# Kernel optimization log

Hardware: AMD Instinct MI355X
Metric: run time of the kernel (lower is better)

The kernel has to match this reference:

```python
import jax, jax.numpy as jnp
import numpy as np

TEMPERATURE = 0.05
EPS = 1e-8  # torch.cosine_similarity eps


def setup_inputs() -> dict:
    key = jax.random.key(0)
    k1, k2 = jax.random.split(key)
    N, D = 8192, 256
    text_embeddings = jax.random.normal(k1, (N, D), dtype=jnp.float32)
    text_pos_embeddings = jax.random.normal(k2, (N, D), dtype=jnp.float32)
    return {"text_embeddings": text_embeddings, "text_pos_embeddings": text_pos_embeddings}


def reference(text_embeddings, text_pos_embeddings):
    # cosine similarity via normalize + single GEMM (same math as broadcasted
    # torch.cosine_similarity, which clamps norms at eps)
    a_norm = jnp.maximum(jnp.linalg.norm(text_embeddings, axis=-1, keepdims=True), EPS)
    b_norm = jnp.maximum(jnp.linalg.norm(text_pos_embeddings, axis=-1, keepdims=True), EPS)
    a = text_embeddings / a_norm  # [N, D]
    b = text_pos_embeddings / b_norm  # [N, D]
    sim = jnp.einsum("nd,md->nm", a, b) / TEMPERATURE  # [N, N]
    # cross-entropy with labels = arange(N): mean over rows of -log_softmax diag
    logp = jax.nn.log_softmax(sim, axis=-1)
    loss = -jnp.mean(jnp.diagonal(logp))
    return loss
```

## Files before the change

kernel.cpp:

```cpp
#include <hip/hip_runtime.h>
#include <hip/hip_bf16.h>
#include <math.h>

#define DIM 256

typedef float f32x4 __attribute__((ext_vector_type(4)));
typedef int   i32x8 __attribute__((ext_vector_type(8)));

__constant__ const float kTempInvLog2e = 20.0f * 1.4426950408889634f;
#define LN2 0.6931471805599453f
#define EPS_NORM 1e-8f
#define SCALE_ONE 0x7F7F7F7Fu

static __device__ inline unsigned f2fp8x4(float4 v, float s) {
    int r = 0;
    r = __builtin_amdgcn_cvt_pk_fp8_f32(v.x * s, v.y * s, r, false);
    r = __builtin_amdgcn_cvt_pk_fp8_f32(v.z * s, v.w * s, r, true);
    return (unsigned)r;
}

static __device__ inline i32x8 ld_frag32(const void* p0, const void* p1) {
    uint4 a = *(const uint4*)p0;
    uint4 b = *(const uint4*)p1;
    i32x8 v;
    v[0] = a.x; v[1] = a.y; v[2] = a.z; v[3] = a.w;
    v[4] = b.x; v[5] = b.y; v[6] = b.z; v[7] = b.w;
    return v;
}

__global__ __launch_bounds__(256) void normpack_kernel(
    const float* __restrict__ A, const float* __restrict__ B,
    unsigned char* __restrict__ Apk, unsigned char* __restrict__ Bpk,
    float* __restrict__ diag, int n)
{
    __shared__ uint4 lA[256];
    __shared__ uint4 lB[256];
    const int t = threadIdx.x;
    const int rl = t >> 4;
    const int c16 = t & 15;
    const int r = blockIdx.x * 16 + rl;

    const float4* pa = (const float4*)(A + (size_t)r * DIM + c16 * 16);
    const float4* pb = (const float4*)(B + (size_t)r * DIM + c16 * 16);
    float4 a0 = pa[0], a1 = pa[1], a2 = pa[2], a3 = pa[3];
    float4 b0 = pb[0], b1 = pb[1], b2 = pb[2], b3 = pb[3];

    float ssa = a0.x*a0.x + a0.y*a0.y + a0.z*a0.z + a0.w*a0.w
              + a1.x*a1.x + a1.y*a1.y + a1.z*a1.z + a1.w*a1.w
              + a2.x*a2.x + a2.y*a2.y + a2.z*a2.z + a2.w*a2.w
              + a3.x*a3.x + a3.y*a3.y + a3.z*a3.z + a3.w*a3.w;
    float ssb = b0.x*b0.x + b0.y*b0.y + b0.z*b0.z + b0.w*b0.w
              + b1.x*b1.x + b1.y*b1.y + b1.z*b1.z + b1.w*b1.w
              + b2.x*b2.x + b2.y*b2.y + b2.z*b2.z + b2.w*b2.w
              + b3.x*b3.x + b3.y*b3.y + b3.z*b3.z + b3.w*b3.w;
    float dd  = a0.x*b0.x + a0.y*b0.y + a0.z*b0.z + a0.w*b0.w
              + a1.x*b1.x + a1.y*b1.y + a1.z*b1.z + a1.w*b1.w
              + a2.x*b2.x + a2.y*b2.y + a2.z*b2.z + a2.w*b2.w
              + a3.x*b3.x + a3.y*b3.y + a3.z*b3.z + a3.w*b3.w;
#pragma unroll
    for (int m = 1; m < 16; m <<= 1) {
        ssa += __shfl_xor(ssa, m, 64);
        ssb += __shfl_xor(ssb, m, 64);
        dd  += __shfl_xor(dd, m, 64);
    }
    float na = fmaxf(sqrtf(ssa), EPS_NORM);
    float nb = fmaxf(sqrtf(ssb), EPS_NORM);
    float sa = kTempInvLog2e / na;
    float sb = 1.0f / nb;
    if (c16 == 0) diag[r] = dd / (na * nb) * kTempInvLog2e;

    const int u = ((c16 >> 3) << 7) + ((c16 & 1) << 6) + rl + ((c16 & 7) >> 1) * 16;
    uint4 ga, gb;
    ga.x = f2fp8x4(a0, sa); ga.y = f2fp8x4(a1, sa);
    ga.z = f2fp8x4(a2, sa); ga.w = f2fp8x4(a3, sa);
    gb.x = f2fp8x4(b0, sb); gb.y = f2fp8x4(b1, sb);
    gb.z = f2fp8x4(b2, sb); gb.w = f2fp8x4(b3, sb);
    lA[u] = ga; lB[u] = gb;
    __syncthreads();

    ((uint4*)Apk)[(size_t)blockIdx.x * 256 + t] = lA[t];
    ((uint4*)Bpk)[(size_t)blockIdx.x * 256 + t] = lB[t];
}

static __device__ inline void async_copy16(const void* g, void* l) {
    __builtin_amdgcn_global_load_lds(
        (const __attribute__((address_space(1))) unsigned int*)g,
        (__attribute__((address_space(3))) unsigned int*)l, 16, 0, 0);
}

__global__ __launch_bounds__(256, 2) void gemm_lse_kernel(
    const unsigned char* __restrict__ Apk, const unsigned char* __restrict__ Bpk,
    float* __restrict__ partial, int n)
{
    __shared__ char ldsbuf[32768];
    const int lane = threadIdx.x & 63;
    const int w = threadIdx.x >> 6;
    const int c = lane & 15;
    const int q = lane >> 4;

    const int i = blockIdx.x;
    const int split = ((i & 7) << 1) | ((i >> 3) & 1);
    const int rowblk = i >> 4;
    const int rowbase = rowblk * 256 + w * 64;

    i32x8 afrag[4][2];
#pragma unroll
    for (int m = 0; m < 4; ++m) {
        const int AT = rowblk * 16 + w * 4 + m;
#pragma unroll
        for (int kc = 0; kc < 2; ++kc) {
            const char* base = (const char*)Apk + ((size_t)AT * 2 + kc) * 2048 + lane * 16;
            afrag[m][kc] = ld_frag32(base, base + 1024);
        }
    }
#pragma unroll
    for (int m = 0; m < 4; ++m)
#pragma unroll
        for (int kc = 0; kc < 2; ++kc)
            asm volatile("" : "+v"(afrag[m][kc]));

    float sums[16];
#pragma unroll
    for (int s = 0; s < 16; ++s) sums[s] = 0.0f;

    const char* bbase = (const char*)Bpk + (size_t)split * 32 * 4096;
    const int niter = 8;

    {
        const char* src = bbase + w * 4096 + (size_t)lane * 16;
        char* dst = ldsbuf + w * 4096;
#pragma unroll
        for (int j = 0; j < 4; ++j)
            async_copy16(src + j * 1024, dst + j * 1024);
    }
    __syncthreads();

    for (int it = 0; it < niter; ++it) {
        const int cur = it & 1;
        if (it + 1 < niter) {
            const char* src = bbase + (size_t)(it + 1) * 16384 + w * 4096 + (size_t)lane * 16;
            char* dst = ldsbuf + (cur ^ 1) * 16384 + w * 4096;
#pragma unroll
            for (int j = 0; j < 4; ++j)
                async_copy16(src + j * 1024, dst + j * 1024);
        }

        f32x4 acc[4][4];
#pragma unroll
        for (int m = 0; m < 4; ++m)
#pragma unroll
            for (int nc = 0; nc < 4; ++nc)
                acc[m][nc] = (f32x4){0.f, 0.f, 0.f, 0.f};

        const char* lb = ldsbuf + cur * 16384 + (size_t)lane * 16;
#pragma unroll
        for (int nc = 0; nc < 4; ++nc) {
#pragma unroll
            for (int kc = 0; kc < 2; ++kc) {
                const char* p = lb + nc * 4096 + kc * 2048;
                i32x8 bfrag = ld_frag32(p, p + 1024);
#pragma unroll
                for (int m = 0; m < 4; ++m)
                    acc[m][nc] = __builtin_amdgcn_mfma_scale_f32_16x16x128_f8f6f4(
                        afrag[m][kc], bfrag, acc[m][nc],
                        0, 0,
                        0, SCALE_ONE,
                        0, SCALE_ONE);
            }
        }

#pragma unroll
        for (int m = 0; m < 4; ++m)
#pragma unroll
            for (int nc = 0; nc < 4; ++nc)
#pragma unroll
                for (int r = 0; r < 4; ++r)
                    sums[m * 4 + r] += __builtin_amdgcn_exp2f(acc[m][nc][r]);

        __syncthreads();
    }

#pragma unroll
    for (int s = 0; s < 16; ++s) {
        float v = sums[s];
        v += __shfl_xor(v, 1, 64);
        v += __shfl_xor(v, 2, 64);
        v += __shfl_xor(v, 4, 64);
        v += __shfl_xor(v, 8, 64);
        sums[s] = v;
    }
    if (c == 0) {
#pragma unroll
        for (int m = 0; m < 4; ++m)
#pragma unroll
            for (int r = 0; r < 4; ++r)
                partial[(size_t)(rowbase + m * 16 + q * 4 + r) * 16 + split] = sums[m * 4 + r];
    }
}

__global__ __launch_bounds__(1024) void finale_kernel(
    const float* __restrict__ partial, const float* __restrict__ diag,
    float* __restrict__ out, int n)
{
    __shared__ float red[1024];
    float local = 0.0f;
    for (int row = threadIdx.x; row < n; row += 1024) {
        const float4* p = (const float4*)(partial + (size_t)row * 16);
        float4 p0 = p[0], p1 = p[1], p2 = p[2], p3 = p[3];
        float s = (p0.x + p0.y + p0.z + p0.w) + (p1.x + p1.y + p1.z + p1.w)
                + (p2.x + p2.y + p2.z + p2.w) + (p3.x + p3.y + p3.z + p3.w);
        local += log2f(s) - diag[row];
    }
    red[threadIdx.x] = local;
    __syncthreads();
    for (int off = 512; off > 0; off >>= 1) {
        if (threadIdx.x < off) red[threadIdx.x] += red[threadIdx.x + off];
        __syncthreads();
    }
    if (threadIdx.x == 0) out[0] = red[0] * (LN2 / (float)n);
}

extern "C" void kernel_launch(void* const* d_in, const int* in_sizes, int n_in,
                              void* d_out, int out_size, void* d_ws, size_t ws_size,
                              hipStream_t stream) {
    const int n = in_sizes[0] / DIM;
    const float* A = (const float*)d_in[0];
    const float* B = (const float*)d_in[1];
    float* out = (float*)d_out;

    unsigned char* Apk = (unsigned char*)d_ws;
    unsigned char* Bpk = Apk + (size_t)n * DIM;
    float* partial = (float*)(Bpk + (size_t)n * DIM);
    float* diag = partial + (size_t)n * 16;

    normpack_kernel<<<n / 16, 256, 0, stream>>>(A, B, Apk, Bpk, diag, n);

    gemm_lse_kernel<<<(n / 256) * 16, 256, 0, stream>>>(Apk, Bpk, partial, n);

    finale_kernel<<<1, 1024, 0, stream>>>(partial, diag, out, n);
}
```

Before: 96.22 us.

## Split columns into 32 blocks, load whole B tile into LDS once

The GEMM grid is doubled so each block covers 256 columns instead of 512. The block copies its full 64KB B slice into LDS with a single async load and one barrier, replacing the double-buffered loop with its per-iteration syncs. The A-fragment loads are issued after the B copy so the two overlap. This gives more blocks and fewer barriers, at the cost of 64KB LDS per block, which may cap occupancy at 2 blocks per CU, and a wider partial buffer for the finale to reduce.

```diff
diff --git a/kernel.cpp b/kernel.cpp
--- a/kernel.cpp
+++ b/kernel.cpp
@@ -92,16 +92,24 @@
     const unsigned char* __restrict__ Apk, const unsigned char* __restrict__ Bpk,
     float* __restrict__ partial, int n)
 {
-    __shared__ char ldsbuf[32768];
+    __shared__ char ldsbuf[65536];
     const int lane = threadIdx.x & 63;
     const int w = threadIdx.x >> 6;
     const int c = lane & 15;
     const int q = lane >> 4;
 
     const int i = blockIdx.x;
-    const int split = ((i & 7) << 1) | ((i >> 3) & 1);
-    const int rowblk = i >> 4;
+    const int colblk = ((i & 7) << 2) | ((i >> 3) & 3);
+    const int rowblk = i >> 5;
     const int rowbase = rowblk * 256 + w * 64;
+
+    {
+        const char* src = (const char*)Bpk + (size_t)colblk * 65536 + w * 16384 + (size_t)lane * 16;
+        char* dst = ldsbuf + w * 16384;
+#pragma unroll
+        for (int j = 0; j < 16; ++j)
+            async_copy16(src + j * 1024, dst + j * 1024);
+    }
 
     i32x8 afrag[4][2];
 #pragma unroll
@@ -123,61 +131,31 @@
 #pragma unroll
     for (int s = 0; s < 16; ++s) sums[s] = 0.0f;
 
-    const char* bbase = (const char*)Bpk + (size_t)split * 32 * 4096;
-    const int niter = 8;
-
-    {
-        const char* src = bbase + w * 4096 + (size_t)lane * 16;
-        char* dst = ldsbuf + w * 4096;
-#pragma unroll
-        for (int j = 0; j < 4; ++j)
-            async_copy16(src + j * 1024, dst + j * 1024);
-    }
     __syncthreads();
 
-    for (int it = 0; it < niter; ++it) {
-        const int cur = it & 1;
-        if (it + 1 < niter) {
-            const char* src = bbase + (size_t)(it + 1) * 16384 + w * 4096 + (size_t)lane * 16;
-            char* dst = ldsbuf + (cur ^ 1) * 16384 + w * 4096;
-#pragma unroll
-            for (int j = 0; j < 4; ++j)
-                async_copy16(src + j * 1024, dst + j * 1024);
+    const char* lb = ldsbuf + (size_t)lane * 16;
+#pragma unroll 4
+    for (int nc = 0; nc < 16; ++nc) {
+        f32x4 acc[4];
+#pragma unroll
+        for (int m = 0; m < 4; ++m) acc[m] = (f32x4){0.f, 0.f, 0.f, 0.f};
+#pragma unroll
+        for (int kc = 0; kc < 2; ++kc) {
+            const char* p = lb + nc * 4096 + kc * 2048;
+            i32x8 bfrag = ld_frag32(p, p + 1024);
+#pragma unroll
+            for (int m = 0; m < 4; ++m)
+                acc[m] = __builtin_amdgcn_mfma_scale_f32_16x16x128_f8f6f4(
+                    afrag[m][kc], bfrag, acc[m],
+                    0, 0,
+                    0, SCALE_ONE,
+                    0, SCALE_ONE);
         }
-
-        f32x4 acc[4][4];
 #pragma unroll
         for (int m = 0; m < 4; ++m)
 #pragma unroll
-            for (int nc = 0; nc < 4; ++nc)
-                acc[m][nc] = (f32x4){0.f, 0.f, 0.f, 0.f};
-
-        const char* lb = ldsbuf + cur * 16384 + (size_t)lane * 16;
-#pragma unroll
-        for (int nc = 0; nc < 4; ++nc) {
-#pragma unroll
-            for (int kc = 0; kc < 2; ++kc) {
-                const char* p = lb + nc * 4096 + kc * 2048;
-                i32x8 bfrag = ld_frag32(p, p + 1024);
-#pragma unroll
-                for (int m = 0; m < 4; ++m)
-                    acc[m][nc] = __builtin_amdgcn_mfma_scale_f32_16x16x128_f8f6f4(
-                        afrag[m][kc], bfrag, acc[m][nc],
-                        0, 0,
-                        0, SCALE_ONE,
-                        0, SCALE_ONE);
-            }
-        }
-
-#pragma unroll
-        for (int m = 0; m < 4; ++m)
-#pragma unroll
-            for (int nc = 0; nc < 4; ++nc)
-#pragma unroll
-                for (int r = 0; r < 4; ++r)
-                    sums[m * 4 + r] += __builtin_amdgcn_exp2f(acc[m][nc][r]);
-
-        __syncthreads();
+            for (int r = 0; r < 4; ++r)
+                sums[m * 4 + r] += __builtin_amdgcn_exp2f(acc[m][r]);
     }
 
 #pragma unroll
@@ -194,7 +172,7 @@
         for (int m = 0; m < 4; ++m)
 #pragma unroll
             for (int r = 0; r < 4; ++r)
-                partial[(size_t)(rowbase + m * 16 + q * 4 + r) * 16 + split] = sums[m * 4 + r];
+                partial[(size_t)(rowbase + m * 16 + q * 4 + r) * 32 + colblk] = sums[m * 4 + r];
     }
 }
 
@@ -205,10 +183,13 @@
     __shared__ float red[1024];
     float local = 0.0f;
     for (int row = threadIdx.x; row < n; row += 1024) {
-        const float4* p = (const float4*)(partial + (size_t)row * 16);
-        float4 p0 = p[0], p1 = p[1], p2 = p[2], p3 = p[3];
-        float s = (p0.x + p0.y + p0.z + p0.w) + (p1.x + p1.y + p1.z + p1.w)
-                + (p2.x + p2.y + p2.z + p2.w) + (p3.x + p3.y + p3.z + p3.w);
+        const float4* p = (const float4*)(partial + (size_t)row * 32);
+        float s = 0.0f;
+#pragma unroll
+        for (int j = 0; j < 8; ++j) {
+            float4 v = p[j];
+            s += (v.x + v.y) + (v.z + v.w);
+        }
         local += log2f(s) - diag[row];
     }
     red[threadIdx.x] = local;
@@ -231,11 +212,11 @@
     unsigned char* Apk = (unsigned char*)d_ws;
     unsigned char* Bpk = Apk + (size_t)n * DIM;
     float* partial = (float*)(Bpk + (size_t)n * DIM);
-    float* diag = partial + (size_t)n * 16;
+    float* diag = partial + (size_t)n * 32;
 
     normpack_kernel<<<n / 16, 256, 0, stream>>>(A, B, Apk, Bpk, diag, n);
 
-    gemm_lse_kernel<<<(n / 256) * 16, 256, 0, stream>>>(Apk, Bpk, partial, n);
+    gemm_lse_kernel<<<(n / 256) * 32, 256, 0, stream>>>(Apk, Bpk, partial, n);
 
     finale_kernel<<<1, 1024, 0, stream>>>(partial, diag, out, n);
 }
```

New measurement: 115.9 us. 20.4% more time.
